# Optimization experiments

Hardware: AMD Instinct MI355X
Metric: run time of the kernel (lower is better)

The kernel has to match this reference:

```python
import jax, jax.numpy as jnp
import numpy as np
import math

N_EMBD = 1024
NUM_HEADS = 16
MAX_LEN = 2048
AUX = 256
B, T = 2, 2048


def setup_inputs() -> dict:
    key = jax.random.key(0)
    ks = jax.random.split(key, 16)
    s = 0.02
    C, A = N_EMBD, AUX
    inp = {
        "x": jax.random.normal(ks[0], (B, T, C), jnp.float32),
        "aux_x": jax.random.normal(ks[1], (B, T, A), jnp.float32),
        "Wq": s * jax.random.normal(ks[2], (C, C), jnp.float32),
        "bq": jnp.zeros((C,), jnp.float32),
        "Wk": s * jax.random.normal(ks[3], (C + A, C), jnp.float32),
        "bk": jnp.zeros((C,), jnp.float32),
        "Wv": s * jax.random.normal(ks[4], (C + A, C), jnp.float32),
        "bv": jnp.zeros((C,), jnp.float32),
        "Wo": s * jax.random.normal(ks[5], (C, C), jnp.float32),  # zero-init in source; randomized for a meaningful baseline
        "bo": jnp.zeros((C,), jnp.float32),
        "PEq": s * jax.random.normal(ks[6], (MAX_LEN, C), jnp.float32),
        "PEk": s * jax.random.normal(ks[7], (MAX_LEN, C), jnp.float32),
        "attn_mask": jax.random.bernoulli(ks[8], 0.9, (B, T, T)),
        "frame_indices": jax.random.randint(ks[9], (B, T), 0, MAX_LEN),
        "num_heads": NUM_HEADS,
    }
    return inp


def reference(x, aux_x, Wq, bq, Wk, bk, Wv, bv, Wo, bo, PEq, PEk, attn_mask, frame_indices, num_heads):
    Bx, Tx, C = x.shape
    H = num_heads
    hd = C // H
    x_aug = jnp.concatenate([x, aux_x], axis=2)  # [B,T,C+A]
    # QKV projections, split heads; PE added per (position, head) to q and k
    q = (x @ Wq + bq).reshape(Bx, Tx, H, hd) + PEq[frame_indices].reshape(Bx, Tx, H, hd)
    k = (x_aug @ Wk + bk).reshape(Bx, Tx, H, hd) + PEk[frame_indices].reshape(Bx, Tx, H, hd)
    v = (x_aug @ Wv + bv).reshape(Bx, Tx, H, hd)
    scale = 1.0 / math.sqrt(hd)
    scores = jnp.einsum("bqhd,bkhd->bhqk", q, k) * scale  # [B,H,T,T]
    scores = jnp.where(attn_mask[:, None, :, :], scores, -jnp.inf)
    attn = jax.nn.softmax(scores, axis=-1)  # fully-masked rows -> NaN
    out = jnp.einsum("bhqk,bkhd->bqhd", attn, v).reshape(Bx, Tx, C)
    out = jnp.nan_to_num(out, nan=0.0)
    return out @ Wo + bo
```

## Files before the change

kernel.cpp:

```cpp
#include <hip/hip_runtime.h>
#include <hip/hip_bf16.h>

typedef unsigned short u16;
typedef unsigned int u32;
typedef __attribute__((ext_vector_type(8))) short bf16x8;
typedef __attribute__((ext_vector_type(4))) float f32x4;

#define HD 64
#define NH 16
#define TT 2048
#define BB 2
#define CA 1280

__device__ __forceinline__ u16 bfu(float f) {
    u32 u = __builtin_bit_cast(u32, f);
    u32 r = u + 0x7fffu + ((u >> 16) & 1u);
    return (u16)(r >> 16);
}

__device__ __forceinline__ float ex2(float x) {
#if __has_builtin(__builtin_amdgcn_exp2f)
    return __builtin_amdgcn_exp2f(x);
#else
    return exp2f(x);
#endif
}

__device__ __forceinline__ void gload16(const void* g, void* l) {
    __builtin_amdgcn_global_load_lds(
        (const __attribute__((address_space(1))) unsigned int*)g,
        (__attribute__((address_space(3))) unsigned int*)l,
        16, 0, 0);
}

__global__ void build_xaug(const float* __restrict__ x, const float* __restrict__ aux,
                           u16* __restrict__ xa) {
    int i = blockIdx.x * 256 + threadIdx.x;
    int row = i / 320;
    int c4 = i - row * 320;
    float4 v;
    if (c4 < 256) v = ((const float4*)x)[row * 256 + c4];
    else          v = ((const float4*)aux)[row * 64 + (c4 - 256)];
    u16 o0 = bfu(v.x), o1 = bfu(v.y), o2 = bfu(v.z), o3 = bfu(v.w);
    ushort4 pk; pk.x = o0; pk.y = o1; pk.z = o2; pk.w = o3;
    ((ushort4*)xa)[i] = pk;
}

__global__ void wtrans(const float* __restrict__ src, u16* __restrict__ dst,
                       int Ksrc, int Kpad, int Nsrc) {
    __shared__ float tile[32][33];
    int kt = blockIdx.x * 32, nt = blockIdx.y * 32;
    int r = threadIdx.x >> 5, c = threadIdx.x & 31;
    #pragma unroll
    for (int i = 0; i < 4; i++) {
        int k = kt + r + i * 8;
        tile[r + i * 8][c] = (k < Ksrc) ? src[(size_t)k * Nsrc + nt + c] : 0.f;
    }
    __syncthreads();
    #pragma unroll
    for (int i = 0; i < 4; i++) {
        int n = nt + r + i * 8;
        dst[(size_t)n * Kpad + kt + c] = bfu(tile[c][r + i * 8]);
    }
}

__global__ void pack_mask(const unsigned char* __restrict__ m, u32* __restrict__ bits) {
    __shared__ u32 modeSh;
    if (threadIdx.x == 0) modeSh = 0;
    __syncthreads();
    const u32* wp = (const u32*)m;
    u32 local = 0;
    for (int j = threadIdx.x; j < 2048; j += 256) {
        u32 v = wp[j];
        if (v == 0x3f800000u) local |= 2u;
        else if (v > 1u) local |= 1u;
        if ((j & 1) && v != 0u) local |= 4u;
    }
    if (local) atomicOr(&modeSh, local);
    __syncthreads();
    u32 mode = modeSh;
    bool words32 = (mode & 2u) || (mode == 4u);
    bool bytes8 = !words32 && (mode & 1u);

    int i = blockIdx.x * 256 + threadIdx.x;
    size_t e0 = (size_t)i * 32;
    u32 r = 0;
    if (words32) {
        const uint4* q = (const uint4*)(wp + e0);
        #pragma unroll
        for (int j4 = 0; j4 < 8; j4++) {
            uint4 v = q[j4];
            if (v.x) r |= 1u << (j4 * 4 + 0);
            if (v.y) r |= 1u << (j4 * 4 + 1);
            if (v.z) r |= 1u << (j4 * 4 + 2);
            if (v.w) r |= 1u << (j4 * 4 + 3);
        }
    } else if (bytes8) {
        const unsigned char* p = m + e0;
        uint4 a = *(const uint4*)p;
        uint4 b = *(const uint4*)(p + 16);
        u32 words[8] = {a.x, a.y, a.z, a.w, b.x, b.y, b.z, b.w};
        #pragma unroll
        for (int jw = 0; jw < 8; jw++) {
            u32 x = words[jw];
            r |= ((x >> 0) & 1u) << (jw * 4 + 0);
            r |= ((x >> 8) & 1u) << (jw * 4 + 1);
            r |= ((x >> 16) & 1u) << (jw * 4 + 2);
            r |= ((x >> 24) & 1u) << (jw * 4 + 3);
        }
    } else {
        #pragma unroll 4
        for (int j = 0; j < 32; j++)
            if (wp[(e0 + j) * 2]) r |= 1u << j;
    }
    bits[i] = r;
}

__global__ void vtrans(const u16* __restrict__ v, u16* __restrict__ vt) {
    __shared__ u16 tile[64][72];
    int bh = blockIdx.y;
    int t0 = blockIdx.x * 64;
    int tid = threadIdx.x;
    int r = tid >> 3;
    int c = (tid & 7) * 8;
    const u16* src = v + ((size_t)bh * TT + t0) * HD;
    *(uint4*)&tile[r][c]      = *(const uint4*)&src[r * HD + c];
    *(uint4*)&tile[r + 32][c] = *(const uint4*)&src[(r + 32) * HD + c];
    __syncthreads();
    u16* dst = vt + (size_t)bh * HD * TT + t0;
    #pragma unroll
    for (int ii = 0; ii < 2; ii++) {
        int dd = r + ii * 32;
        u16 tmp[8];
        #pragma unroll
        for (int j = 0; j < 8; j++) tmp[j] = tile[c + j][dd];
        *(uint4*)&dst[(size_t)dd * TT + c] = *(const uint4*)tmp;
    }
}

template <int MODE>
__global__ __launch_bounds__(256, 3) void gemm_bt(
    const u16* __restrict__ A, const u16* __restrict__ Bt, int K,
    const float* __restrict__ biasq, const float* __restrict__ biask,
    const float* __restrict__ biasv, const float* __restrict__ PEq,
    const float* __restrict__ PEk, const int* __restrict__ fidx,
    u16* __restrict__ qo, u16* __restrict__ ko, u16* __restrict__ vo,
    float* __restrict__ fo, const float* __restrict__ bo) {
    __shared__ u16 As[128 * 64];
    __shared__ u16 Bs[128 * 64];
    const int tid = threadIdx.x, lane = tid & 63, w = tid >> 6;
    const int l15 = lane & 15, l4 = lane >> 4;
    const int wm = w >> 1, wn = w & 1;
    const int bm = blockIdx.x, bn = blockIdx.y;

    f32x4 acc[4][4] = {};

    const int srow = lane >> 3;
    const int schunk = (lane & 7) ^ srow;
    const u16* ag = A + (size_t)(bm * 128 + w * 32 + srow) * K + schunk * 8;
    const u16* bg = Bt + (size_t)(bn * 128 + w * 32 + srow) * K + schunk * 8;
    u16* asl = &As[(w * 32) * 64] + lane * 8;
    u16* bsl = &Bs[(w * 32) * 64] + lane * 8;

    for (int kt = 0; kt < K; kt += 64) {
        #pragma unroll
        for (int i = 0; i < 4; i++) {
            gload16(ag + (size_t)i * 8 * K + kt, asl + i * 8 * 64);
            gload16(bg + (size_t)i * 8 * K + kt, bsl + i * 8 * 64);
        }
        __syncthreads();
        #pragma unroll
        for (int ks = 0; ks < 2; ks++) {
            bf16x8 af[4], bfr[4];
            #pragma unroll
            for (int mi = 0; mi < 4; mi++) {
                int row = wm * 64 + mi * 16 + l15;
                af[mi] = *(const bf16x8*)&As[row * 64 + (((ks * 4 + l4) ^ (row & 7)) * 8)];
            }
            #pragma unroll
            for (int ni = 0; ni < 4; ni++) {
                int row = wn * 64 + ni * 16 + l15;
                bfr[ni] = *(const bf16x8*)&Bs[row * 64 + (((ks * 4 + l4) ^ (row & 7)) * 8)];
            }
            #pragma unroll
            for (int mi = 0; mi < 4; mi++)
                #pragma unroll
                for (int ni = 0; ni < 4; ni++)
                    acc[mi][ni] = __builtin_amdgcn_mfma_f32_16x16x32_bf16(
                        af[mi], bfr[ni], acc[mi][ni], 0, 0, 0);
        }
        __syncthreads();
    }

    if (MODE == 0) {
        #pragma unroll
        for (int mi = 0; mi < 4; mi++) {
            #pragma unroll
            for (int r = 0; r < 4; r++) {
                int m = bm * 128 + wm * 64 + mi * 16 + l4 * 4 + r;
                int b = m >> 11, t = m & 2047;
                int fi = fidx[m];
                #pragma unroll
                for (int ni = 0; ni < 4; ni++) {
                    int ng = bn * 128 + wn * 64 + ni * 16 + l15;
                    int sec = ng >> 10, nn = ng & 1023;
                    float val = acc[mi][ni][r];
                    size_t oidx = ((size_t)(b * NH + (nn >> 6)) * TT + t) * HD + (nn & 63);
                    if (sec == 0) {
                        val += biasq[nn] + PEq[(size_t)fi * 1024 + nn];
                        val *= 0.180336880111120419f;
                        qo[oidx] = bfu(val);
                    } else if (sec == 1) {
                        val += biask[nn] + PEk[(size_t)fi * 1024 + nn];
                        ko[oidx] = bfu(val);
                    } else {
                        val += biasv[nn];
                        vo[oidx] = bfu(val);
                    }
                }
            }
        }
    } else {
        #pragma unroll
        for (int mi = 0; mi < 4; mi++) {
            #pragma unroll
            for (int r = 0; r < 4; r++) {
                int m = bm * 128 + wm * 64 + mi * 16 + l4 * 4 + r;
                #pragma unroll
                for (int ni = 0; ni < 4; ni++) {
                    int ng = bn * 128 + wn * 64 + ni * 16 + l15;
                    fo[(size_t)m * 1024 + ng] = acc[mi][ni][r] + bo[ng];
                }
            }
        }
    }
}

__global__ __launch_bounds__(256, 4) void attn_fwd(
    const u16* __restrict__ Q, const u16* __restrict__ Kg,
    const u16* __restrict__ VT, const u32* __restrict__ mbits,
    u16* __restrict__ Og) {
    __shared__ u16 KPs[64 * 136];
    __shared__ u16 Vs[64 * 128];
    const int tid = threadIdx.x, lane = tid & 63, w = tid >> 6;
    const int l15 = lane & 15, l4 = lane >> 4;
    const int qt = blockIdx.x, bh = blockIdx.y;
    const int b = bh >> 4;
    const size_t hoff = (size_t)bh * (TT * HD);

    bf16x8 qf[2];
    {
        int qbase = qt * 64 + w * 16;
        #pragma unroll
        for (int ks = 0; ks < 2; ks++)
            qf[ks] = *(const bf16x8*)&Q[hoff + (size_t)(qbase + l15) * HD + ks * 32 + l4 * 8];
    }

    bf16x8 ones;
    #pragma unroll
    for (int j = 0; j < 8; j++) ones[j] = (short)0x3F80;

    f32x4 po[4] = {};
    f32x4 pol = {};

    const int srow = lane >> 3;
    const int schunk = (lane & 7) ^ srow;
    const u16* kgl = Kg + hoff + (size_t)(w * 32 + srow) * HD + schunk * 8;
    u16* ksl = &KPs[(w * 32) * 64] + lane * 8;
    const size_t voff = (size_t)bh * (HD * TT);
    const size_t mbase = ((size_t)(b * TT + qt * 64 + w * 16 + l4 * 4)) * 64;
    const int shEven = 31 - l15, shOdd = 15 - l15;

    for (int kt = 0; kt < 16; kt++) {
        uint4 mb[4];
        #pragma unroll
        for (int r = 0; r < 4; r++)
            mb[r] = *(const uint4*)&mbits[mbase + (size_t)r * 64 + kt * 4];

        #pragma unroll
        for (int i = 0; i < 4; i++)
            gload16(kgl + (size_t)(kt * 128 + i * 8) * HD, ksl + i * 8 * 64);
        #pragma unroll
        for (int i = 0; i < 4; i++) {
            int d = w * 16 + i * 4 + l4;
            const u16* src = VT + voff + (size_t)d * TT + kt * 128 + ((l15 ^ (d & 15)) * 8);
            gload16(src, &Vs[(w * 16 + i * 4) * 128] + lane * 8);
        }
        __syncthreads();

        f32x4 s[8];
        __builtin_amdgcn_s_setprio(1);
        #pragma unroll
        for (int nt = 0; nt < 8; nt++) {
            int krow = nt * 16 + l15;
            bf16x8 kf0 = *(const bf16x8*)&KPs[krow * 64 + (((0 + l4) ^ (krow & 7)) * 8)];
            bf16x8 kf1 = *(const bf16x8*)&KPs[krow * 64 + (((4 + l4) ^ (krow & 7)) * 8)];
            f32x4 z = {0.f, 0.f, 0.f, 0.f};
            z = __builtin_amdgcn_mfma_f32_16x16x32_bf16(qf[0], kf0, z, 0, 0, 0);
            s[nt] = __builtin_amdgcn_mfma_f32_16x16x32_bf16(qf[1], kf1, z, 0, 0, 0);
        }
        __builtin_amdgcn_s_setprio(0);
        __syncthreads();

        #pragma unroll
        for (int r = 0; r < 4; r++) {
            u32 mw0 = mb[r].x, mw1 = mb[r].y, mw2 = mb[r].z, mw3 = mb[r].w;
            u32 mw[4] = {mw0, mw1, mw2, mw3};
            int prow = w * 16 + l4 * 4 + r;
            u16* pw = &KPs[prow * 136 + l15];
            #pragma unroll
            for (int nt = 0; nt < 8; nt++) {
                u32 word = mw[nt >> 1];
                int sh = (nt & 1) ? shOdd : shEven;
                u32 ext = (u32)(((int)(word << sh)) >> 31);
                float p = ex2(s[nt][r]);
                u32 pb = __builtin_bit_cast(u32, p) & ext;
                pw[nt * 16] = (u16)(pb >> 16);
            }
        }

        bf16x8 pf[4];
        #pragma unroll
        for (int ks = 0; ks < 4; ks++)
            pf[ks] = *(const bf16x8*)&KPs[(w * 16 + l15) * 136 + ks * 32 + l4 * 8];
        __builtin_amdgcn_s_setprio(1);
        #pragma unroll
        for (int nto = 0; nto < 4; nto++) {
            #pragma unroll
            for (int ks = 0; ks < 4; ks++) {
                int d = nto * 16 + l15;
                bf16x8 vf = *(const bf16x8*)&Vs[d * 128 + (((ks * 4 + l4) ^ (d & 15)) * 8)];
                po[nto] = __builtin_amdgcn_mfma_f32_16x16x32_bf16(
                    pf[ks], vf, po[nto], 0, 0, 0);
            }
        }
        #pragma unroll
        for (int ks = 0; ks < 4; ks++)
            pol = __builtin_amdgcn_mfma_f32_16x16x32_bf16(pf[ks], ones, pol, 0, 0, 0);
        __builtin_amdgcn_s_setprio(0);
        __syncthreads();
    }

    int h = bh & 15;
    #pragma unroll
    for (int r = 0; r < 4; r++) {
        float lv = pol[r];
        float inv = (lv > 0.f) ? (1.f / lv) : 0.f;
        int t = qt * 64 + w * 16 + l4 * 4 + r;
        #pragma unroll
        for (int nto = 0; nto < 4; nto++)
            Og[((size_t)(b * TT + t)) * 1024 + h * 64 + nto * 16 + l15] =
                bfu(po[nto][r] * inv);
    }
}

extern "C" void kernel_launch(void* const* d_in, const int* in_sizes, int n_in,
                              void* d_out, int out_size, void* d_ws, size_t ws_size,
                              hipStream_t stream) {
    const float* x   = (const float*)d_in[0];
    const float* aux = (const float*)d_in[1];
    const float* Wq  = (const float*)d_in[2];
    const float* bq  = (const float*)d_in[3];
    const float* Wk  = (const float*)d_in[4];
    const float* bk  = (const float*)d_in[5];
    const float* Wv  = (const float*)d_in[6];
    const float* bv  = (const float*)d_in[7];
    const float* Wo  = (const float*)d_in[8];
    const float* bo  = (const float*)d_in[9];
    const float* PEq = (const float*)d_in[10];
    const float* PEk = (const float*)d_in[11];
    const unsigned char* mask = (const unsigned char*)d_in[12];
    const int* fidx  = (const int*)d_in[13];
    float* out = (float*)d_out;

    char* ws = (char*)d_ws;
    u16* XA    = (u16*)(ws + 0);
    u16* AttO  = (u16*)(ws + 0);
    u16* WTall = (u16*)(ws + 10485760);
    u16* WTo   = (u16*)(ws + 18350080);
    u16* Qb    = (u16*)(ws + 20447232);
    u16* Kb    = (u16*)(ws + 28835840);
    u16* Vb    = (u16*)(ws + 37224448);
    u16* VTb   = (u16*)(ws + 45613056);
    u32* MB    = (u32*)(ws + 54001664);

    build_xaug<<<5120, 256, 0, stream>>>(x, aux, XA);
    wtrans<<<dim3(40, 32), 256, 0, stream>>>(Wq, WTall, 1024, 1280, 1024);
    wtrans<<<dim3(40, 32), 256, 0, stream>>>(Wk, WTall + (size_t)1024 * 1280, 1280, 1280, 1024);
    wtrans<<<dim3(40, 32), 256, 0, stream>>>(Wv, WTall + (size_t)2048 * 1280, 1280, 1280, 1024);
    wtrans<<<dim3(32, 32), 256, 0, stream>>>(Wo, WTo, 1024, 1024, 1024);
    pack_mask<<<1024, 256, 0, stream>>>(mask, MB);

    gemm_bt<0><<<dim3(32, 24), 256, 0, stream>>>(
        XA, WTall, 1280, bq, bk, bv, PEq, PEk, fidx, Qb, Kb, Vb, nullptr, nullptr);

    vtrans<<<dim3(32, 32), 256, 0, stream>>>(Vb, VTb);

    attn_fwd<<<dim3(32, 32), 256, 0, stream>>>(Qb, Kb, VTb, MB, AttO);

    gemm_bt<1><<<dim3(32, 8), 256, 0, stream>>>(
        AttO, WTo, 1024, nullptr, nullptr, nullptr, nullptr, nullptr, nullptr,
        nullptr, nullptr, nullptr, out, bo);
}
```

Baseline: 174.5 us.

## Split QK^T by key columns per wave and merge weight-transpose launches

In the attention kernel each wave now computes scores for all 64 query rows over its own 32-key slice, where before it covered 16 query rows against all 128 keys. The Q fragments are held in registers for all four row blocks, so each K fragment is read from LDS once and reused four times. The mask bit-packing layout is transposed to match the new per-wave access pattern, and an extra barrier is added before the P·V stage because P rows are now written by several waves. The four weight-transpose launches are merged into one 3D grid to cut launch overhead, at the cost of more Q registers per thread and one more sync per key tile.

```diff
diff --git a/kernel.cpp b/kernel.cpp
--- a/kernel.cpp
+++ b/kernel.cpp
@@ -46,15 +46,23 @@
     ((ushort4*)xa)[i] = pk;
 }
 
-__global__ void wtrans(const float* __restrict__ src, u16* __restrict__ dst,
-                       int Ksrc, int Kpad, int Nsrc) {
+__global__ void wtrans_all(const float* __restrict__ Wq, const float* __restrict__ Wk,
+                           const float* __restrict__ Wv, const float* __restrict__ Wo,
+                           u16* __restrict__ WTall, u16* __restrict__ WTo) {
+    int z = blockIdx.z;
+    const float* src = (z == 0) ? Wq : (z == 1) ? Wk : (z == 2) ? Wv : Wo;
+    u16* dst = (z == 3) ? WTo : WTall + (size_t)z * 1024 * 1280;
+    int Ksrc = (z == 0 || z == 3) ? 1024 : 1280;
+    int Kpad = (z == 3) ? 1024 : 1280;
+    int kt = blockIdx.x * 32;
+    if (kt >= Kpad) return;
     __shared__ float tile[32][33];
-    int kt = blockIdx.x * 32, nt = blockIdx.y * 32;
+    int nt = blockIdx.y * 32;
     int r = threadIdx.x >> 5, c = threadIdx.x & 31;
     #pragma unroll
     for (int i = 0; i < 4; i++) {
         int k = kt + r + i * 8;
-        tile[r + i * 8][c] = (k < Ksrc) ? src[(size_t)k * Nsrc + nt + c] : 0.f;
+        tile[r + i * 8][c] = (k < Ksrc) ? src[(size_t)k * 1024 + nt + c] : 0.f;
     }
     __syncthreads();
     #pragma unroll
@@ -82,8 +90,11 @@
     bool words32 = (mode & 2u) || (mode == 4u);
     bool bytes8 = !words32 && (mode & 1u);
 
-    int i = blockIdx.x * 256 + threadIdx.x;
-    size_t e0 = (size_t)i * 32;
+    int j = blockIdx.x * 256 + threadIdx.x;
+    int b = j >> 17;
+    int word = (j >> 11) & 63;
+    int t = j & 2047;
+    size_t e0 = ((size_t)(b * 2048 + t)) * 2048 + word * 32;
     u32 r = 0;
     if (words32) {
         const uint4* q = (const uint4*)(wp + e0);
@@ -98,8 +109,8 @@
     } else if (bytes8) {
         const unsigned char* p = m + e0;
         uint4 a = *(const uint4*)p;
-        uint4 b = *(const uint4*)(p + 16);
-        u32 words[8] = {a.x, a.y, a.z, a.w, b.x, b.y, b.z, b.w};
+        uint4 bwords = *(const uint4*)(p + 16);
+        u32 words[8] = {a.x, a.y, a.z, a.w, bwords.x, bwords.y, bwords.z, bwords.w};
         #pragma unroll
         for (int jw = 0; jw < 8; jw++) {
             u32 x = words[jw];
@@ -110,10 +121,10 @@
         }
     } else {
         #pragma unroll 4
-        for (int j = 0; j < 32; j++)
-            if (wp[(e0 + j) * 2]) r |= 1u << j;
-    }
-    bits[i] = r;
+        for (int jj = 0; jj < 32; jj++)
+            if (wp[(e0 + jj) * 2]) r |= 1u << jj;
+    }
+    bits[((size_t)(b * 64 + word) << 11) | t] = r;
 }
 
 __global__ void vtrans(const u16* __restrict__ v, u16* __restrict__ vt) {
@@ -248,13 +259,12 @@
     const int b = bh >> 4;
     const size_t hoff = (size_t)bh * (TT * HD);
 
-    bf16x8 qf[2];
-    {
-        int qbase = qt * 64 + w * 16;
+    bf16x8 qf[4][2];
+    #pragma unroll
+    for (int mi = 0; mi < 4; mi++)
         #pragma unroll
         for (int ks = 0; ks < 2; ks++)
-            qf[ks] = *(const bf16x8*)&Q[hoff + (size_t)(qbase + l15) * HD + ks * 32 + l4 * 8];
-    }
+            qf[mi][ks] = *(const bf16x8*)&Q[hoff + (size_t)(qt * 64 + mi * 16 + l15) * HD + ks * 32 + l4 * 8];
 
     bf16x8 ones;
     #pragma unroll
@@ -268,14 +278,14 @@
     const u16* kgl = Kg + hoff + (size_t)(w * 32 + srow) * HD + schunk * 8;
     u16* ksl = &KPs[(w * 32) * 64] + lane * 8;
     const size_t voff = (size_t)bh * (HD * TT);
-    const size_t mbase = ((size_t)(b * TT + qt * 64 + w * 16 + l4 * 4)) * 64;
+    const u32* mbp = mbits + ((size_t)b * 64) * TT + qt * 64;
     const int shEven = 31 - l15, shOdd = 15 - l15;
 
     for (int kt = 0; kt < 16; kt++) {
         uint4 mb[4];
         #pragma unroll
-        for (int r = 0; r < 4; r++)
-            mb[r] = *(const uint4*)&mbits[mbase + (size_t)r * 64 + kt * 4];
+        for (int mi = 0; mi < 4; mi++)
+            mb[mi] = *(const uint4*)&mbp[(size_t)(kt * 4 + w) * TT + mi * 16 + l4 * 4];
 
         #pragma unroll
         for (int i = 0; i < 4; i++)
@@ -288,36 +298,39 @@
         }
         __syncthreads();
 
-        f32x4 s[8];
+        f32x4 s[4][2];
         __builtin_amdgcn_s_setprio(1);
         #pragma unroll
-        for (int nt = 0; nt < 8; nt++) {
-            int krow = nt * 16 + l15;
+        for (int ntl = 0; ntl < 2; ntl++) {
+            int krow = w * 32 + ntl * 16 + l15;
             bf16x8 kf0 = *(const bf16x8*)&KPs[krow * 64 + (((0 + l4) ^ (krow & 7)) * 8)];
             bf16x8 kf1 = *(const bf16x8*)&KPs[krow * 64 + (((4 + l4) ^ (krow & 7)) * 8)];
-            f32x4 z = {0.f, 0.f, 0.f, 0.f};
-            z = __builtin_amdgcn_mfma_f32_16x16x32_bf16(qf[0], kf0, z, 0, 0, 0);
-            s[nt] = __builtin_amdgcn_mfma_f32_16x16x32_bf16(qf[1], kf1, z, 0, 0, 0);
+            #pragma unroll
+            for (int mi = 0; mi < 4; mi++) {
+                f32x4 z = {0.f, 0.f, 0.f, 0.f};
+                z = __builtin_amdgcn_mfma_f32_16x16x32_bf16(qf[mi][0], kf0, z, 0, 0, 0);
+                s[mi][ntl] = __builtin_amdgcn_mfma_f32_16x16x32_bf16(qf[mi][1], kf1, z, 0, 0, 0);
+            }
         }
         __builtin_amdgcn_s_setprio(0);
         __syncthreads();
 
         #pragma unroll
-        for (int r = 0; r < 4; r++) {
-            u32 mw0 = mb[r].x, mw1 = mb[r].y, mw2 = mb[r].z, mw3 = mb[r].w;
-            u32 mw[4] = {mw0, mw1, mw2, mw3};
-            int prow = w * 16 + l4 * 4 + r;
-            u16* pw = &KPs[prow * 136 + l15];
-            #pragma unroll
-            for (int nt = 0; nt < 8; nt++) {
-                u32 word = mw[nt >> 1];
-                int sh = (nt & 1) ? shOdd : shEven;
-                u32 ext = (u32)(((int)(word << sh)) >> 31);
-                float p = ex2(s[nt][r]);
-                u32 pb = __builtin_bit_cast(u32, p) & ext;
-                pw[nt * 16] = (u16)(pb >> 16);
-            }
-        }
+        for (int mi = 0; mi < 4; mi++) {
+            u32 wr[4] = {mb[mi].x, mb[mi].y, mb[mi].z, mb[mi].w};
+            #pragma unroll
+            for (int ntl = 0; ntl < 2; ntl++) {
+                int sh = ntl ? shOdd : shEven;
+                #pragma unroll
+                for (int r = 0; r < 4; r++) {
+                    u32 ext = (u32)(((int)(wr[r] << sh)) >> 31);
+                    float p = ex2(s[mi][ntl][r]);
+                    u32 pb = __builtin_bit_cast(u32, p) & ext;
+                    KPs[(mi * 16 + l4 * 4 + r) * 136 + w * 32 + ntl * 16 + l15] = (u16)(pb >> 16);
+                }
+            }
+        }
+        __syncthreads();
 
         bf16x8 pf[4];
         #pragma unroll
@@ -385,10 +398,7 @@
     u32* MB    = (u32*)(ws + 54001664);
 
     build_xaug<<<5120, 256, 0, stream>>>(x, aux, XA);
-    wtrans<<<dim3(40, 32), 256, 0, stream>>>(Wq, WTall, 1024, 1280, 1024);
-    wtrans<<<dim3(40, 32), 256, 0, stream>>>(Wk, WTall + (size_t)1024 * 1280, 1280, 1280, 1024);
-    wtrans<<<dim3(40, 32), 256, 0, stream>>>(Wv, WTall + (size_t)2048 * 1280, 1280, 1280, 1024);
-    wtrans<<<dim3(32, 32), 256, 0, stream>>>(Wo, WTo, 1024, 1024, 1024);
+    wtrans_all<<<dim3(40, 32, 4), 256, 0, stream>>>(Wq, Wk, Wv, Wo, WTall, WTo);
     pack_mask<<<1024, 256, 0, stream>>>(mask, MB);
 
     gemm_bt<0><<<dim3(32, 24), 256, 0, stream>>>(
```

After: 186.0 us. 6.5% more time.

## Split K and P shared buffers to drop a barrier; merge weight transposes

Applied to the files above, without the earlier changes.

The attention kernel now keeps K and P in separate shared-memory buffers, so one __syncthreads between the QK^T MFMAs and the P writes can be removed. The extra shared memory lowers the launch-bounds occupancy hint from 4 to 3 blocks per CU. The four weight-transpose launches are also merged into one 3D-grid launch, with early exit for out-of-range tiles, to cut launch overhead. Lower occupancy may reduce latency hiding in attention.

```diff
diff --git a/kernel.cpp b/kernel.cpp
--- a/kernel.cpp
+++ b/kernel.cpp
@@ -46,15 +46,23 @@
     ((ushort4*)xa)[i] = pk;
 }
 
-__global__ void wtrans(const float* __restrict__ src, u16* __restrict__ dst,
-                       int Ksrc, int Kpad, int Nsrc) {
+__global__ void wtrans_all(const float* __restrict__ Wq, const float* __restrict__ Wk,
+                           const float* __restrict__ Wv, const float* __restrict__ Wo,
+                           u16* __restrict__ WTall, u16* __restrict__ WTo) {
+    int z = blockIdx.z;
+    const float* src = (z == 0) ? Wq : (z == 1) ? Wk : (z == 2) ? Wv : Wo;
+    u16* dst = (z == 3) ? WTo : WTall + (size_t)z * 1024 * 1280;
+    int Ksrc = (z == 0 || z == 3) ? 1024 : 1280;
+    int Kpad = (z == 3) ? 1024 : 1280;
+    int kt = blockIdx.x * 32;
+    if (kt >= Kpad) return;
     __shared__ float tile[32][33];
-    int kt = blockIdx.x * 32, nt = blockIdx.y * 32;
+    int nt = blockIdx.y * 32;
     int r = threadIdx.x >> 5, c = threadIdx.x & 31;
     #pragma unroll
     for (int i = 0; i < 4; i++) {
         int k = kt + r + i * 8;
-        tile[r + i * 8][c] = (k < Ksrc) ? src[(size_t)k * Nsrc + nt + c] : 0.f;
+        tile[r + i * 8][c] = (k < Ksrc) ? src[(size_t)k * 1024 + nt + c] : 0.f;
     }
     __syncthreads();
     #pragma unroll
@@ -236,12 +244,13 @@
     }
 }
 
-__global__ __launch_bounds__(256, 4) void attn_fwd(
+__global__ __launch_bounds__(256, 3) void attn_fwd(
     const u16* __restrict__ Q, const u16* __restrict__ Kg,
     const u16* __restrict__ VT, const u32* __restrict__ mbits,
     u16* __restrict__ Og) {
-    __shared__ u16 KPs[64 * 136];
+    __shared__ u16 Ks[128 * 64];
     __shared__ u16 Vs[64 * 128];
+    __shared__ u16 Ps[64 * 136];
     const int tid = threadIdx.x, lane = tid & 63, w = tid >> 6;
     const int l15 = lane & 15, l4 = lane >> 4;
     const int qt = blockIdx.x, bh = blockIdx.y;
@@ -266,7 +275,7 @@
     const int srow = lane >> 3;
     const int schunk = (lane & 7) ^ srow;
     const u16* kgl = Kg + hoff + (size_t)(w * 32 + srow) * HD + schunk * 8;
-    u16* ksl = &KPs[(w * 32) * 64] + lane * 8;
+    u16* ksl = &Ks[(w * 32) * 64] + lane * 8;
     const size_t voff = (size_t)bh * (HD * TT);
     const size_t mbase = ((size_t)(b * TT + qt * 64 + w * 16 + l4 * 4)) * 64;
     const int shEven = 31 - l15, shOdd = 15 - l15;
@@ -293,21 +302,19 @@
         #pragma unroll
         for (int nt = 0; nt < 8; nt++) {
             int krow = nt * 16 + l15;
-            bf16x8 kf0 = *(const bf16x8*)&KPs[krow * 64 + (((0 + l4) ^ (krow & 7)) * 8)];
-            bf16x8 kf1 = *(const bf16x8*)&KPs[krow * 64 + (((4 + l4) ^ (krow & 7)) * 8)];
+            bf16x8 kf0 = *(const bf16x8*)&Ks[krow * 64 + (((0 + l4) ^ (krow & 7)) * 8)];
+            bf16x8 kf1 = *(const bf16x8*)&Ks[krow * 64 + (((4 + l4) ^ (krow & 7)) * 8)];
             f32x4 z = {0.f, 0.f, 0.f, 0.f};
             z = __builtin_amdgcn_mfma_f32_16x16x32_bf16(qf[0], kf0, z, 0, 0, 0);
             s[nt] = __builtin_amdgcn_mfma_f32_16x16x32_bf16(qf[1], kf1, z, 0, 0, 0);
         }
         __builtin_amdgcn_s_setprio(0);
-        __syncthreads();
 
         #pragma unroll
         for (int r = 0; r < 4; r++) {
-            u32 mw0 = mb[r].x, mw1 = mb[r].y, mw2 = mb[r].z, mw3 = mb[r].w;
-            u32 mw[4] = {mw0, mw1, mw2, mw3};
+            u32 mw[4] = {mb[r].x, mb[r].y, mb[r].z, mb[r].w};
             int prow = w * 16 + l4 * 4 + r;
-            u16* pw = &KPs[prow * 136 + l15];
+            u16* pw = &Ps[prow * 136 + l15];
             #pragma unroll
             for (int nt = 0; nt < 8; nt++) {
                 u32 word = mw[nt >> 1];
@@ -322,7 +329,7 @@
         bf16x8 pf[4];
         #pragma unroll
         for (int ks = 0; ks < 4; ks++)
-            pf[ks] = *(const bf16x8*)&KPs[(w * 16 + l15) * 136 + ks * 32 + l4 * 8];
+            pf[ks] = *(const bf16x8*)&Ps[(w * 16 + l15) * 136 + ks * 32 + l4 * 8];
         __builtin_amdgcn_s_setprio(1);
         #pragma unroll
         for (int nto = 0; nto < 4; nto++) {
@@ -385,10 +392,7 @@
     u32* MB    = (u32*)(ws + 54001664);
 
     build_xaug<<<5120, 256, 0, stream>>>(x, aux, XA);
-    wtrans<<<dim3(40, 32), 256, 0, stream>>>(Wq, WTall, 1024, 1280, 1024);
-    wtrans<<<dim3(40, 32), 256, 0, stream>>>(Wk, WTall + (size_t)1024 * 1280, 1280, 1280, 1024);
-    wtrans<<<dim3(40, 32), 256, 0, stream>>>(Wv, WTall + (size_t)2048 * 1280, 1280, 1280, 1024);
-    wtrans<<<dim3(32, 32), 256, 0, stream>>>(Wo, WTo, 1024, 1024, 1024);
+    wtrans_all<<<dim3(40, 32, 4), 256, 0, stream>>>(Wq, Wk, Wv, Wo, WTall, WTo);
     pack_mask<<<1024, 256, 0, stream>>>(mask, MB);
 
     gemm_bt<0><<<dim3(32, 24), 256, 0, stream>>>(
```

After: 178.2 us. 2.1% more time.
